# Optimization experiments

Hardware: AMD Instinct MI355X
Metric: run time of the kernel (lower is better)

The kernel has to match this reference:

```python
import jax, jax.numpy as jnp
import numpy as np

DELTA = 0.05
STOP = 10
INV_DELTA = 1.0 / DELTA
TOTAL = int(STOP * INV_DELTA)  # 200 bins
# slice_vol = arange(delta/2, stop, delta)**1 * delta * 2*pi*3
SLICE_VOL = (np.arange(DELTA / 2, STOP, DELTA) * DELTA * 2.0 * np.pi * 3.0).astype(np.float32)


def _cdist(a, b):
    # Euclidean pairwise distance [Na, Nb] via the (a-b)^2 = a^2 + b^2 - 2ab identity
    a2 = jnp.sum(a * a, axis=-1)
    b2 = jnp.sum(b * b, axis=-1)
    d2 = a2[:, None] + b2[None, :] - 2.0 * (a @ b.T)
    return jnp.sqrt(jnp.maximum(d2, 0.0))


def _pair_hist(pa, pb, same, real_size, vol):
    # integer distance bins; torch .int() truncates, distances are >= 0 so floor is equivalent
    bins = jnp.floor(_cdist(pa * real_size, pb * real_size) * INV_DELTA).astype(jnp.int32)
    if same:
        n = pa.shape[0]
        idx = jnp.arange(n)
        bins = bins.at[idx, idx].set(9999)  # fill_diagonal_(9999) -> excluded self-pairs
    valid = (bins < TOTAL).astype(jnp.float32).ravel()  # mask: bins beyond stop dropped
    counts = jnp.zeros(TOTAL, jnp.float32).at[jnp.clip(bins, 0, TOTAL - 1).ravel()].add(valid)
    density = pb.shape[0] / vol
    return counts / density / jnp.asarray(SLICE_VOL) / pa.shape[0]


def setup_inputs() -> dict:
    key = jax.random.key(0)
    k0, k1 = jax.random.split(key)
    pos0 = jax.random.uniform(k0, (4096, 3), dtype=jnp.float32)
    pos1 = jax.random.uniform(k1, (8192, 3), dtype=jnp.float32)
    count = jnp.zeros((2, 2, TOTAL), dtype=jnp.float32)
    real_size = jnp.array([25.0, 25.0, 3.0], dtype=jnp.float32)
    return {"pos0": pos0, "pos1": pos1, "count": count, "real_size": real_size}


def reference(pos0, pos1, count, real_size):
    vol = real_size[0] * real_size[1] * real_size[2]
    pos = [pos0, pos1]
    bufs = [
        jnp.stack([_pair_hist(pos[i], pos[j], i == j, real_size, vol) for j in range(2)])
        for i in range(2)
    ]
    # count buffer is accumulated in-place in torch; return the updated buffer
    return count + jnp.stack(bufs)
```

## Files before the change

### kernel.cpp

```cpp
#include <hip/hip_runtime.h>
#include <math.h>

#define TOTAL 200
#define TB    128
#define BLK   256
#define NH    8

__global__ void rdf_prep(const float* __restrict__ p0, const float* __restrict__ p1,
                         const float* __restrict__ rs,
                         float4* __restrict__ b0, float4* __restrict__ b1,
                         unsigned int* __restrict__ hist, int n0, int n1)
{
    const float sx = rs[0], sy = rs[1], sz = rs[2];
    int t = blockIdx.x * blockDim.x + threadIdx.x;
    if (t < n0) {
        float x = p0[t*3+0]*sx, y = p0[t*3+1]*sy, z = p0[t*3+2]*sz;
        b0[t] = make_float4(x, y, z, x*x + y*y + z*z);
    } else if (t < n0 + n1) {
        int u = t - n0;
        float x = p1[u*3+0]*sx, y = p1[u*3+1]*sy, z = p1[u*3+2]*sz;
        b1[u] = make_float4(x, y, z, x*x + y*y + z*z);
    }
    if (blockIdx.x == 0)
        for (int k = threadIdx.x; k < 3*TOTAL; k += BLK) hist[k] = 0;
}

template<bool DIAG>
__device__ __forceinline__ void pair_loop(const float4* __restrict__ Bs,
                                          float ax, float ay, float az, float a2,
                                          unsigned int* __restrict__ mylh, int ofs)
{
    #pragma unroll 8
    for (int j = 0; j < TB; ++j) {
        float4 b  = Bs[j];
        float dot = ax*b.x + ay*b.y + az*b.z;
        float d2  = (a2 + b.w) - 2.0f*dot;
        float v   = __builtin_amdgcn_sqrtf(fmaxf(d2, 0.0f)) * 20.0f;
        bool ok   = (v < 200.0f);
        if (DIAG) ok = ok && (j > ofs);
        if (ok) atomicAdd(&mylh[(int)v], 1u);
    }
}

__global__ __launch_bounds__(BLK) void rdf_hist(
    const float4* __restrict__ b0, const float4* __restrict__ b1,
    unsigned int* __restrict__ hist,
    int n0, int n1, int p0, int p01, int cb0, int cb1)
{
    __shared__ unsigned int lh[NH][TOTAL];

    int bid = blockIdx.x;
    const float4* Abase; const float4* Bbase;
    int nA, histIdx, nCols; bool self;
    if (bid < p0)       { Abase=b0; Bbase=b0; nA=n0; histIdx=0; self=true;  nCols=cb0; }
    else if (bid < p01) { Abase=b0; Bbase=b1; nA=n0; histIdx=1; self=false; nCols=cb1; bid -= p0; }
    else                { Abase=b1; Bbase=b1; nA=n1; histIdx=2; self=true;  nCols=cb1; bid -= p01; }
    int rb = bid / nCols;
    int cb = bid % nCols;

    const int rowBase = rb * BLK;
    const int colBase = cb * TB;
    if (self && (colBase + TB - 1) < rowBase) return;
    const bool diag = self && (colBase < rowBase + BLK);

    const int tid  = threadIdx.x;
    const int wave = tid >> 6;
    unsigned int* mylh = &lh[(wave << 1) | (tid & 1)][0];

    for (int k = tid; k < NH*TOTAL; k += BLK) ((unsigned int*)lh)[k] = 0;
    __syncthreads();

    const int  aIdx   = rowBase + tid;
    const bool aValid = aIdx < nA;
    const float4* Bs  = Bbase + colBase;

    if (aValid) {
        float4 a = Abase[aIdx];
        if (diag) pair_loop<true >(Bs, a.x, a.y, a.z, a.w, mylh, aIdx - colBase);
        else      pair_loop<false>(Bs, a.x, a.y, a.z, a.w, mylh, 0);
    }
    __syncthreads();

    for (int k = tid; k < TOTAL; k += BLK) {
        unsigned int c = 0;
        #pragma unroll
        for (int h = 0; h < NH; ++h) c += lh[h][k];
        if (c) atomicAdd(&hist[histIdx*TOTAL + k], self ? 2u*c : c);
    }
}

__global__ void rdf_final(const unsigned int* __restrict__ hist,
                          const float* __restrict__ count,
                          const float* __restrict__ rs,
                          float* __restrict__ out, int n0, int n1)
{
    int t = blockIdx.x * blockDim.x + threadIdx.x;
    if (t >= 2*2*TOTAL) return;
    int k = t % TOTAL;
    int j = (t / TOTAL) & 1;
    int i = t / (2*TOTAL);

    float vol = rs[0]*rs[1]*rs[2];
    int Na = (i == 0) ? n0 : n1;
    int Nb = (j == 0) ? n0 : n1;
    int hidx = (i == j) ? (i == 0 ? 0 : 2) : 1;

    float c = (float)hist[hidx*TOTAL + k];
    double sv  = ((0.025 + (double)k * 0.05) * 0.05) * 2.0 * M_PI * 3.0;
    float  svf = (float)sv;
    float  density = (float)Nb / vol;
    float  r = ((c / density) / svf) / (float)Na;
    out[t] = count[t] + r;
}

extern "C" void kernel_launch(void* const* d_in, const int* in_sizes, int n_in,
                              void* d_out, int out_size, void* d_ws, size_t ws_size,
                              hipStream_t stream) {
    const float* pos0  = (const float*)d_in[0];
    const float* pos1  = (const float*)d_in[1];
    const float* count = (const float*)d_in[2];
    const float* rs    = (const float*)d_in[3];
    float* out = (float*)d_out;

    int n0 = in_sizes[0] / 3;
    int n1 = in_sizes[1] / 3;

    unsigned int* hist = (unsigned int*)d_ws;
    float4* b0 = (float4*)((char*)d_ws + 4096);
    float4* b1 = b0 + n0;

    int prepBlocks = (n0 + n1 + BLK - 1) / BLK;
    rdf_prep<<<prepBlocks, BLK, 0, stream>>>(pos0, pos1, rs, b0, b1, hist, n0, n1);

    int rb0 = (n0 + BLK - 1) / BLK;
    int rb1 = (n1 + BLK - 1) / BLK;
    int cb0 = (n0 + TB - 1) / TB;
    int cb1 = (n1 + TB - 1) / TB;
    int p0  = rb0 * cb0;
    int p1  = rb0 * cb1;
    int p2  = rb1 * cb1;

    rdf_hist<<<p0 + p1 + p2, BLK, 0, stream>>>(b0, b1, hist,
                                               n0, n1, p0, p0 + p1, cb0, cb1);

    rdf_final<<<(2*2*TOTAL + BLK - 1) / BLK, BLK, 0, stream>>>(hist, count, rs, out, n0, n1);
}
```

Baseline: 119.0 us.

## Use fixed persistent grid over compacted triangular tiles with replicated global histograms

Replaces the one-block-per-tile launch, which spawned many early-exit blocks for the lower triangle, with a fixed grid of 2048 blocks. Each block walks a contiguous range of only the valid tiles, using closed-form triangular indexing, and keeps per-type shared histograms across tiles. Column tiles shrink from 128 to 32 and global atomics are spread over 16 replicated histograms that the final kernel sums. This aims to balance load and cut wasted blocks and atomic contention, at the cost of a serial row search per tile and more per-tile overhead from the smaller tiles.

```diff
diff --git a/kernel.cpp b/kernel.cpp
--- a/kernel.cpp
+++ b/kernel.cpp
@@ -2,14 +2,17 @@
 #include <math.h>
 
 #define TOTAL 200
-#define TB    128
+#define TB    32
 #define BLK   256
-#define NH    8
+#define NW    4
+#define GRID  2048
+#define NR    16
+#define RATIO (BLK/TB)
 
 __global__ void rdf_prep(const float* __restrict__ p0, const float* __restrict__ p1,
                          const float* __restrict__ rs,
                          float4* __restrict__ b0, float4* __restrict__ b1,
-                         unsigned int* __restrict__ hist, int n0, int n1)
+                         unsigned int* __restrict__ ghist, int n0, int n1)
 {
     const float sx = rs[0], sy = rs[1], sz = rs[2];
     int t = blockIdx.x * blockDim.x + threadIdx.x;
@@ -21,8 +24,7 @@
         float x = p1[u*3+0]*sx, y = p1[u*3+1]*sy, z = p1[u*3+2]*sz;
         b1[u] = make_float4(x, y, z, x*x + y*y + z*z);
     }
-    if (blockIdx.x == 0)
-        for (int k = threadIdx.x; k < 3*TOTAL; k += BLK) hist[k] = 0;
+    if (t < NR * 3 * TOTAL) ghist[t] = 0;
 }
 
 template<bool DIAG>
@@ -44,52 +46,67 @@
 
 __global__ __launch_bounds__(BLK) void rdf_hist(
     const float4* __restrict__ b0, const float4* __restrict__ b1,
-    unsigned int* __restrict__ hist,
-    int n0, int n1, int p0, int p01, int cb0, int cb1)
+    unsigned int* __restrict__ ghist,
+    int n0, int n1, int T0, int T01, int Ttot,
+    int cb0, int cb1, int rows0, int rows1)
 {
-    __shared__ unsigned int lh[NH][TOTAL];
-
-    int bid = blockIdx.x;
-    const float4* Abase; const float4* Bbase;
-    int nA, histIdx, nCols; bool self;
-    if (bid < p0)       { Abase=b0; Bbase=b0; nA=n0; histIdx=0; self=true;  nCols=cb0; }
-    else if (bid < p01) { Abase=b0; Bbase=b1; nA=n0; histIdx=1; self=false; nCols=cb1; bid -= p0; }
-    else                { Abase=b1; Bbase=b1; nA=n1; histIdx=2; self=true;  nCols=cb1; bid -= p01; }
-    int rb = bid / nCols;
-    int cb = bid % nCols;
-
-    const int rowBase = rb * BLK;
-    const int colBase = cb * TB;
-    if (self && (colBase + TB - 1) < rowBase) return;
-    const bool diag = self && (colBase < rowBase + BLK);
+    __shared__ unsigned int lh[3][NW][2][TOTAL];
 
     const int tid  = threadIdx.x;
     const int wave = tid >> 6;
-    unsigned int* mylh = &lh[(wave << 1) | (tid & 1)][0];
+    const int par  = tid & 1;
 
-    for (int k = tid; k < NH*TOTAL; k += BLK) ((unsigned int*)lh)[k] = 0;
+    uint4* z = (uint4*)lh;
+    for (int k = tid; k < 3*NW*2*TOTAL/4; k += BLK) z[k] = make_uint4(0,0,0,0);
     __syncthreads();
 
-    const int  aIdx   = rowBase + tid;
-    const bool aValid = aIdx < nA;
-    const float4* Bs  = Bbase + colBase;
+    const int gBeg = (int)(((long long)blockIdx.x       * Ttot) / GRID);
+    const int gEnd = (int)(((long long)(blockIdx.x + 1) * Ttot) / GRID);
 
-    if (aValid) {
-        float4 a = Abase[aIdx];
+    for (int g = gBeg; g < gEnd; ++g) {
+        int type, rb, cb;
+        if (g < T0) {
+            type = 0; rb = 0;
+            while (rb + 1 < rows0 && (cb0*(rb+1) - (RATIO/2)*(rb+1)*rb) <= g) ++rb;
+            cb = RATIO*rb + (g - (cb0*rb - (RATIO/2)*rb*(rb-1)));
+        } else if (g < T01) {
+            int u = g - T0; type = 1; rb = u / cb1; cb = u - rb*cb1;
+        } else {
+            int u = g - T01; type = 2; rb = 0;
+            while (rb + 1 < rows1 && (cb1*(rb+1) - (RATIO/2)*(rb+1)*rb) <= u) ++rb;
+            cb = RATIO*rb + (u - (cb1*rb - (RATIO/2)*rb*(rb-1)));
+        }
+        const float4* Ab = (type == 2) ? b1 : b0;
+        const float4* Bb = (type == 0) ? b0 : b1;
+        const int nA     = (type == 2) ? n1 : n0;
+
+        const int rowBase = rb * BLK;
+        const int colBase = cb * TB;
+        const int aIdx    = rowBase + tid;
+
+        float4 a = (aIdx < nA) ? Ab[aIdx]
+                               : make_float4(0.f, 0.f, 0.f, 3.0e18f);
+        unsigned int* mylh = &lh[type][wave][par][0];
+        const float4* Bs   = Bb + colBase;
+
+        const bool diag = (type != 1) && (colBase < rowBase + BLK);
         if (diag) pair_loop<true >(Bs, a.x, a.y, a.z, a.w, mylh, aIdx - colBase);
         else      pair_loop<false>(Bs, a.x, a.y, a.z, a.w, mylh, 0);
     }
     __syncthreads();
 
-    for (int k = tid; k < TOTAL; k += BLK) {
+    unsigned int* gh = ghist + (blockIdx.x & (NR - 1)) * (3 * TOTAL);
+    for (int k = tid; k < 3 * TOTAL; k += BLK) {
+        int type = k / TOTAL, bin = k - type * TOTAL;
         unsigned int c = 0;
         #pragma unroll
-        for (int h = 0; h < NH; ++h) c += lh[h][k];
-        if (c) atomicAdd(&hist[histIdx*TOTAL + k], self ? 2u*c : c);
+        for (int w = 0; w < NW; ++w)
+            { c += lh[type][w][0][bin] + lh[type][w][1][bin]; }
+        if (c) atomicAdd(&gh[k], (type == 1) ? c : 2u * c);
     }
 }
 
-__global__ void rdf_final(const unsigned int* __restrict__ hist,
+__global__ void rdf_final(const unsigned int* __restrict__ ghist,
                           const float* __restrict__ count,
                           const float* __restrict__ rs,
                           float* __restrict__ out, int n0, int n1)
@@ -105,11 +122,14 @@
     int Nb = (j == 0) ? n0 : n1;
     int hidx = (i == j) ? (i == 0 ? 0 : 2) : 1;
 
-    float c = (float)hist[hidx*TOTAL + k];
+    unsigned int c = 0;
+    #pragma unroll
+    for (int r = 0; r < NR; ++r) c += ghist[r*3*TOTAL + hidx*TOTAL + k];
+
     double sv  = ((0.025 + (double)k * 0.05) * 0.05) * 2.0 * M_PI * 3.0;
     float  svf = (float)sv;
     float  density = (float)Nb / vol;
-    float  r = ((c / density) / svf) / (float)Na;
+    float  r = (((float)c / density) / svf) / (float)Na;
     out[t] = count[t] + r;
 }
 
@@ -125,23 +145,25 @@
     int n0 = in_sizes[0] / 3;
     int n1 = in_sizes[1] / 3;
 
-    unsigned int* hist = (unsigned int*)d_ws;
-    float4* b0 = (float4*)((char*)d_ws + 4096);
+    unsigned int* ghist = (unsigned int*)d_ws;
+    float4* b0 = (float4*)((char*)d_ws + 40960);
     float4* b1 = b0 + n0;
 
     int prepBlocks = (n0 + n1 + BLK - 1) / BLK;
-    rdf_prep<<<prepBlocks, BLK, 0, stream>>>(pos0, pos1, rs, b0, b1, hist, n0, n1);
+    rdf_prep<<<prepBlocks, BLK, 0, stream>>>(pos0, pos1, rs, b0, b1, ghist, n0, n1);
 
-    int rb0 = (n0 + BLK - 1) / BLK;
-    int rb1 = (n1 + BLK - 1) / BLK;
-    int cb0 = (n0 + TB - 1) / TB;
-    int cb1 = (n1 + TB - 1) / TB;
-    int p0  = rb0 * cb0;
-    int p1  = rb0 * cb1;
-    int p2  = rb1 * cb1;
+    int rows0 = (n0 + BLK - 1) / BLK;
+    int rows1 = (n1 + BLK - 1) / BLK;
+    int cb0   = (n0 + TB - 1) / TB;
+    int cb1   = (n1 + TB - 1) / TB;
+    int T0   = cb0*rows0 - (RATIO/2)*rows0*(rows0-1);
+    int Tc   = rows0*cb1;
+    int T2   = cb1*rows1 - (RATIO/2)*rows1*(rows1-1);
+    int T01  = T0 + Tc;
+    int Ttot = T01 + T2;
 
-    rdf_hist<<<p0 + p1 + p2, BLK, 0, stream>>>(b0, b1, hist,
-                                               n0, n1, p0, p0 + p1, cb0, cb1);
+    rdf_hist<<<GRID, BLK, 0, stream>>>(b0, b1, ghist, n0, n1,
+                                       T0, T01, Ttot, cb0, cb1, rows0, rows1);
 
-    rdf_final<<<(2*2*TOTAL + BLK - 1) / BLK, BLK, 0, stream>>>(hist, count, rs, out, n0, n1);
+    rdf_final<<<(2*2*TOTAL + BLK - 1) / BLK, BLK, 0, stream>>>(ghist, count, rs, out, n0, n1);
 }
```

New measurement: 103.7 us, median of 2. 1.15x faster.
